# Kernel optimization log

Hardware: AMD Instinct MI355X
Metric: run time of the kernel (lower is better)

Reference implementation:

```python
import jax, jax.numpy as jnp
import numpy as np

# dims
B, S, E, H = 2, 2048, 2048, 2688   # batch, seq, embedding_dim, hidden_dim
NH, DH = 4, 2688 // 4              # mLSTM heads, head dim
KS = 4                             # causal conv kernel size
BLK = 4                            # qkv_proj_blocksize
NPH = H // BLK                     # headwise-proj heads


def setup_inputs() -> dict:
    key = jax.random.key(0)
    ks = jax.random.split(key, 12)
    r = lambda i, shape, s=0.02: jax.random.normal(ks[i], shape, jnp.float32) * s
    return dict(
        x=jax.random.normal(ks[0], (B, S, E), jnp.float32),
        W_in=r(1, (E, 2 * H)),                       # up projection (no bias)
        conv_w=r(2, (KS, 1, H), 0.1),                # depthwise causal conv kernel (W, I/g, O)
        conv_b=jnp.zeros((H,), jnp.float32),
        Wq=r(3, (NPH, BLK, BLK), 0.3),               # headwise q proj
        Wk=r(4, (NPH, BLK, BLK), 0.3),               # headwise k proj
        Wv=r(5, (NPH, BLK, BLK), 0.3),               # headwise v proj
        W_ig=r(6, (3 * H, NH)),                      # input gate proj
        b_ig=jax.random.normal(ks[7], (NH,), jnp.float32),
        W_fg=r(8, (3 * H, NH)),                      # forget gate proj
        b_fg=jnp.linspace(3.0, 6.0, NH).astype(jnp.float32),
        norm_w=jnp.ones((H,), jnp.float32),          # multi-head layernorm weight
        skip=jnp.ones((H,), jnp.float32),            # learnable skip
        W_out=r(9, (H, E)),                          # down projection
    )


def _headwise(x, W):
    # LinearHeadwiseExpand: (B,S,H) -> (B,S,NPH,BLK) -> einsum -> (B,S,H)
    b, s, _ = x.shape
    xh = x.reshape(b, s, NPH, BLK)
    return jnp.einsum('bshd,hdo->bsho', xh, W).reshape(b, s, -1)


def reference(x, W_in, conv_w, conv_b, Wq, Wk, Wv, W_ig, b_ig, W_fg, b_fg, norm_w, skip, W_out):
    x_inner = x @ W_in                               # (B,S,2H)
    x_m, z = jnp.split(x_inner, 2, axis=-1)
    # depthwise causal conv1d
    xc = jax.lax.conv_general_dilated(
        x_m, conv_w, (1,), [(KS - 1, 0)],
        dimension_numbers=('NWC', 'WIO', 'NWC'), feature_group_count=H) + conv_b
    xca = jax.nn.silu(xc)
    q = _headwise(xca, Wq)
    k = _headwise(xca, Wk)
    v = _headwise(x_m, Wv)
    # ---- mLSTM cell (parallel stabilized form) ----
    qh = q.reshape(B, S, NH, DH).transpose(0, 2, 1, 3)   # (B,NH,S,DH)
    kh = k.reshape(B, S, NH, DH).transpose(0, 2, 1, 3)
    vh = v.reshape(B, S, NH, DH).transpose(0, 2, 1, 3)
    if_in = jnp.concatenate([q, k, v], axis=-1)          # (B,S,3H)
    i_pre = (if_in @ W_ig + b_ig).transpose(0, 2, 1)     # (B,NH,S)
    f_pre = (if_in @ W_fg + b_fg).transpose(0, 2, 1)
    log_fg = jax.nn.log_sigmoid(f_pre)                   # (B,NH,S)
    cs = jnp.cumsum(log_fg, axis=-1)
    # log decay matrix: sum of log forget gates t=j+1..i, causal masked
    dmat = cs[:, :, :, None] - cs[:, :, None, :]         # (B,NH,S,S)
    mask = jnp.tril(jnp.ones((S, S), bool))
    log_D = jnp.where(mask, dmat + i_pre[:, :, None, :], -jnp.inf)
    m = jnp.max(log_D, axis=-1, keepdims=True)           # stabilizer (B,NH,S,1)
    D = jnp.exp(log_D - m)
    qk = jnp.einsum('bnsd,bntd->bnst', qh, kh) / jnp.sqrt(jnp.float32(DH))
    C = qk * D
    n = jnp.maximum(jnp.abs(C.sum(-1, keepdims=True)), jnp.exp(-m))
    h = jnp.einsum('bnst,bntd->bnsd', C / (n + 1e-6), vh)
    # multi-head layernorm over DH, learnable scale over full H
    mu = h.mean(-1, keepdims=True)
    var = h.var(-1, keepdims=True)
    hn = (h - mu) * jax.lax.rsqrt(var + 1e-5)
    hn = hn.transpose(0, 2, 1, 3).reshape(B, S, H) * norm_w
    # ---- gated skip + output ----
    h_skip = hn + skip * xca
    hs = h_skip * jax.nn.silu(z)
    return hs @ W_out
```

## Files before the change

### kernel.cpp

```cpp
#include <hip/hip_runtime.h>

typedef unsigned short u16;
typedef unsigned int u32;
typedef __bf16 bf16x8 __attribute__((ext_vector_type(8)));
typedef float f32x4 __attribute__((ext_vector_type(4)));

#define BB   2
#define SS   2048
#define EE   2048
#define HH   2688
#define NHH  4
#define DHH  672
#define NPHH 672
#define H2   5376
#define H3   8064

__device__ __forceinline__ float b2f(u16 u) {
  union { unsigned int i; float f; } c; c.i = ((unsigned int)u) << 16; return c.f;
}
__device__ __forceinline__ u16 f2b(float f) {
  union { float f; unsigned int i; } c; c.f = f;
  unsigned int i = c.i;
  return (u16)((i + 0x7FFFu + ((i >> 16) & 1u)) >> 16);
}
__device__ __forceinline__ float silu_f(float x) { return x / (1.f + __expf(-x)); }
__device__ __forceinline__ float logsig_f(float f) {
  return (f >= 0.f) ? -log1pf(__expf(-f)) : (f - log1pf(__expf(f)));
}

__device__ __forceinline__ void gl2lds16(const u16* g, u16* s) {
  __builtin_amdgcn_global_load_lds(
      (const __attribute__((address_space(1))) u32*)g,
      (__attribute__((address_space(3))) u32*)s, 16, 0, 0);
}

template <int N> __device__ __forceinline__ void vmwait() {
  asm volatile("s_waitcnt vmcnt(%0)" :: "n"(N) : "memory");
}

template <int MODE, int OUTF32>
__global__ __launch_bounds__(512, 1) void gemm8(
    const u16* __restrict__ A, const u16* __restrict__ Bt, void* __restrict__ Cp,
    int M, int N, int K, int lda, int ldb, int ldc,
    long sAhi, long sAlo, long sBhi, long sBlo, long sChi, long sClo,
    const float* __restrict__ aux1, const float* __restrict__ aux2,
    int auxStride, int causal)
{
  constexpr int SLOT = (128 + 256) * 64;
  __shared__ __align__(16) u16 sm[3 * SLOT];

  int gx = gridDim.x;
  int nwg = gx * gridDim.y;
  int flat = blockIdx.y * gx + blockIdx.x;
  int qq = nwg >> 3, r8 = nwg & 7;
  int xcd = flat & 7, seq = flat >> 3;
  int logical = (xcd < r8 ? xcd * (qq + 1) : r8 * (qq + 1) + (xcd - r8) * qq) + seq;
  int bx = logical % gx, by = logical / gx;
  int m0 = by * 128, n0 = bx * 256;
  if (MODE == 1 && n0 > m0 + 127) return;

  int bz = blockIdx.z, bzh = bz >> 2, bzl = bz & 3;
  A  += bzh * sAhi + bzl * sAlo;
  Bt += bzh * sBhi + bzl * sBlo;
  const float* a1 = aux1 ? aux1 + (long)bz * auxStride : nullptr;
  const float* a2 = aux2 ? aux2 + (long)bz * auxStride : nullptr;
  u16*   C16 = (u16*)Cp + bzh * sChi + bzl * sClo;
  float* C32 = (float*)Cp + bzh * sChi + bzl * sClo;

  int t = threadIdx.x, lane = t & 63, w = t >> 6;
  int l15 = lane & 15, quad = lane >> 4;
  int wr = w >> 2, wc = w & 3;

  int srow = t >> 3;
  int sw8 = ((t & 7) ^ (srow & 7)) * 8;
  const u16* pS[6];
  int dOf[6];
#pragma unroll
  for (int c = 0; c < 2; ++c) {
    pS[c] = A + (long)(m0 + c * 64 + srow) * lda + sw8;
    dOf[c] = c * 4096 + w * 512;
  }
#pragma unroll
  for (int c = 0; c < 4; ++c) {
    pS[2 + c] = Bt + (long)(n0 + c * 64 + srow) * ldb + sw8;
    dOf[2 + c] = 8192 + c * 4096 + w * 512;
  }

  f32x4 acc[4][4];
#pragma unroll
  for (int i = 0; i < 4; i++)
#pragma unroll
    for (int j = 0; j < 4; j++) acc[i][j] = (f32x4){0.f, 0.f, 0.f, 0.f};

  int Keff = (MODE == 2 && causal) ? min(K, m0 + 128) : K;
  int T = Keff >> 6;

  auto STAGE = [&](int slot, int k2, int c) {
    gl2lds16(pS[c] + k2, sm + slot * SLOT + dOf[c]);
  };

  int npre = T < 2 ? T : 2;
  for (int tt = 0; tt < npre; ++tt)
#pragma unroll
    for (int c = 0; c < 6; ++c) STAGE(tt, tt << 6, c);
  if (npre >= 2) vmwait<6>(); else vmwait<0>();
  __builtin_amdgcn_s_barrier();
  __builtin_amdgcn_sched_barrier(0);

  int sl = 0;
  for (int tq = 0; tq < T; ++tq) {
    u16* Sb = sm + sl * SLOT;
    int sl2 = sl + 2; if (sl2 >= 3) sl2 -= 3;
    const bool stg = (tq + 2 < T);
    const int k2 = (tq + 2) << 6;
    int cx = (l15 & 7);

    bf16x8 bfr[4][2], af[2][2];
#pragma unroll
    for (int j = 0; j < 4; ++j)
#pragma unroll
      for (int ks = 0; ks < 2; ++ks)
        bfr[j][ks] = *reinterpret_cast<const bf16x8*>(
            Sb + 8192 + (wc * 64 + j * 16 + l15) * 64 + ((((ks << 2) + quad) ^ cx) << 3));
#pragma unroll
    for (int i = 0; i < 2; ++i)
#pragma unroll
      for (int ks = 0; ks < 2; ++ks)
        af[i][ks] = *reinterpret_cast<const bf16x8*>(
            Sb + (wr * 64 + i * 16 + l15) * 64 + ((((ks << 2) + quad) ^ cx) << 3));
    if (stg) { STAGE(sl2, k2, 0); STAGE(sl2, k2, 1); STAGE(sl2, k2, 2); }
    __builtin_amdgcn_s_barrier();
    asm volatile("s_waitcnt lgkmcnt(0)" ::: "memory");
    __builtin_amdgcn_sched_barrier(0);
    __builtin_amdgcn_s_setprio(1);
#pragma unroll
    for (int i = 0; i < 2; ++i)
#pragma unroll
      for (int j = 0; j < 4; ++j) {
        acc[i][j] = __builtin_amdgcn_mfma_f32_16x16x32_bf16(af[i][0], bfr[j][0], acc[i][j], 0, 0, 0);
        acc[i][j] = __builtin_amdgcn_mfma_f32_16x16x32_bf16(af[i][1], bfr[j][1], acc[i][j], 0, 0, 0);
      }
    __builtin_amdgcn_s_setprio(0);
    __builtin_amdgcn_sched_barrier(0);
    __builtin_amdgcn_s_barrier();

    bf16x8 ag[2][2];
#pragma unroll
    for (int i = 0; i < 2; ++i)
#pragma unroll
      for (int ks = 0; ks < 2; ++ks)
        ag[i][ks] = *reinterpret_cast<const bf16x8*>(
            Sb + (wr * 64 + (i + 2) * 16 + l15) * 64 + ((((ks << 2) + quad) ^ cx) << 3));
    if (stg) { STAGE(sl2, k2, 3); STAGE(sl2, k2, 4); STAGE(sl2, k2, 5); }
    __builtin_amdgcn_s_barrier();
    asm volatile("s_waitcnt lgkmcnt(0)" ::: "memory");
    __builtin_amdgcn_sched_barrier(0);
    __builtin_amdgcn_s_setprio(1);
#pragma unroll
    for (int i = 0; i < 2; ++i)
#pragma unroll
      for (int j = 0; j < 4; ++j) {
        acc[i + 2][j] = __builtin_amdgcn_mfma_f32_16x16x32_bf16(ag[i][0], bfr[j][0], acc[i + 2][j], 0, 0, 0);
        acc[i + 2][j] = __builtin_amdgcn_mfma_f32_16x16x32_bf16(ag[i][1], bfr[j][1], acc[i + 2][j], 0, 0, 0);
      }
    __builtin_amdgcn_s_setprio(0);
    __builtin_amdgcn_sched_barrier(0);
    if (tq + 1 < T) {
      if (stg) vmwait<6>(); else vmwait<0>();
      __builtin_amdgcn_s_barrier();
      __builtin_amdgcn_sched_barrier(0);
    }
    sl = sl + 1; if (sl >= 3) sl = 0;
  }

  const float rs = 0.03857583749f;
#pragma unroll
  for (int i = 0; i < 4; i++) {
#pragma unroll
    for (int j = 0; j < 4; j++) {
      int col = n0 + wc * 64 + j * 16 + l15;
      if (col >= N) continue;
#pragma unroll
      for (int rr = 0; rr < 4; rr++) {
        int row = m0 + wr * 64 + i * 16 + quad * 4 + rr;
        if (row >= M) continue;
        float v = acc[i][j][rr];
        if (MODE == 1) v = (col <= row) ? v * rs * __expf(a1[col] - a2[row]) : 0.f;
        else if (MODE == 2) v = v * a1[row];
        if (OUTF32) C32[(long)row * ldc + col] = v;
        else        C16[(long)row * ldc + col] = f2b(v);
      }
    }
  }
}

template <int BM, int MODE, int OUTF32>
__global__ __launch_bounds__(512, 1) void gemm_p(
    const u16* __restrict__ A, const u16* __restrict__ Bt, void* __restrict__ Cp,
    int M, int N, int K, int lda, int ldb, int ldc,
    long sAhi, long sAlo, long sBhi, long sBlo, long sChi, long sClo,
    const float* __restrict__ aux1, const float* __restrict__ aux2,
    int auxStride, int causal)
{
  constexpr int MFR   = BM / 32;
  constexpr int NPH   = MFR / 2;
  constexpr int SLOT  = (BM + 256) * 32;
  constexpr int ACH   = BM / 128;
  constexpr int LOADS = ACH + 2;
  __shared__ __align__(16) u16 sm[4 * SLOT];

  int gx = gridDim.x;
  int nwg = gx * gridDim.y;
  int flat = blockIdx.y * gx + blockIdx.x;
  int qq = nwg >> 3, r8 = nwg & 7;
  int xcd = flat & 7, seq = flat >> 3;
  int logical = (xcd < r8 ? xcd * (qq + 1) : r8 * (qq + 1) + (xcd - r8) * qq) + seq;
  int bx = logical % gx, by = logical / gx;
  int m0 = by * BM, n0 = bx * 256;
  if (MODE == 1 && n0 > m0 + BM - 1) return;

  int bz = blockIdx.z, bzh = bz >> 2, bzl = bz & 3;
  A  += bzh * sAhi + bzl * sAlo;
  Bt += bzh * sBhi + bzl * sBlo;
  const float* a1 = aux1 ? aux1 + (long)bz * auxStride : nullptr;
  const float* a2 = aux2 ? aux2 + (long)bz * auxStride : nullptr;
  u16*   C16 = (u16*)Cp + bzh * sChi + bzl * sClo;
  float* C32 = (float*)Cp + bzh * sChi + bzl * sClo;

  int t = threadIdx.x, lane = t & 63, w = t >> 6;
  int l15 = lane & 15, quad = lane >> 4;
  int wr = w >> 2, wc = w & 3;

  int srow = t >> 2;
  int swz = (((t & 3) ^ ((t >> 3) & 3)) * 8);
  const u16* pS[LOADS];
  int coff[LOADS];
#pragma unroll
  for (int c = 0; c < ACH; ++c) {
    pS[c] = A + (long)(m0 + c * 128 + srow) * lda + swz;
    coff[c] = c * 4096 + w * 512;
  }
#pragma unroll
  for (int c = 0; c < 2; ++c) {
    pS[ACH + c] = Bt + (long)(n0 + c * 128 + srow) * ldb + swz;
    coff[ACH + c] = BM * 32 + c * 4096 + w * 512;
  }

  int rswz = (quad ^ ((l15 >> 1) & 3)) * 8;
  int aoff = (wr * (BM / 2) + l15) * 32 + rswz;
  int boff = BM * 32 + (wc * 64 + l15) * 32 + rswz;

  f32x4 acc[MFR][4];
#pragma unroll
  for (int i = 0; i < MFR; i++)
#pragma unroll
    for (int j = 0; j < 4; j++) acc[i][j] = (f32x4){0.f, 0.f, 0.f, 0.f};

  int Keff = (MODE == 2 && causal) ? min(K, m0 + BM) : K;
  int T = Keff >> 5;

  auto STAGE1 = [&](int tt, int c) {
    gl2lds16(pS[c] + (tt << 5), sm + (tt & 3) * SLOT + coff[c]);
  };

  int npre = T < 3 ? T : 3;
  for (int tt = 0; tt < npre; ++tt)
#pragma unroll
    for (int c = 0; c < LOADS; ++c) STAGE1(tt, c);
  if (npre >= 3)      vmwait<2 * LOADS>();
  else if (npre == 2) vmwait<LOADS>();
  else                vmwait<0>();
  __builtin_amdgcn_s_barrier();
  __builtin_amdgcn_sched_barrier(0);

  for (int tq = 0; tq < T; ++tq) {
    u16* Sb = sm + (tq & 3) * SLOT;
    const bool stg = (tq + 3 < T);
    bf16x8 bf[4];
#pragma unroll
    for (int p = 0; p < NPH; ++p) {
      bf16x8 a0 = *reinterpret_cast<const bf16x8*>(Sb + aoff + (2 * p) * 512);
      bf16x8 a1v = *reinterpret_cast<const bf16x8*>(Sb + aoff + (2 * p + 1) * 512);
      if (p == 0) {
#pragma unroll
        for (int j = 0; j < 4; ++j)
          bf[j] = *reinterpret_cast<const bf16x8*>(Sb + boff + j * 512);
      }
      if (stg) {
#pragma unroll
        for (int c = p * LOADS / NPH; c < (p + 1) * LOADS / NPH; ++c)
          STAGE1(tq + 3, c);
      }
      __builtin_amdgcn_s_barrier();
      asm volatile("s_waitcnt lgkmcnt(0)" ::: "memory");
      __builtin_amdgcn_sched_barrier(0);
      __builtin_amdgcn_s_setprio(1);
#pragma unroll
      for (int j = 0; j < 4; ++j)
        acc[2 * p][j] = __builtin_amdgcn_mfma_f32_16x16x32_bf16(a0, bf[j], acc[2 * p][j], 0, 0, 0);
#pragma unroll
      for (int j = 0; j < 4; ++j)
        acc[2 * p + 1][j] = __builtin_amdgcn_mfma_f32_16x16x32_bf16(a1v, bf[j], acc[2 * p + 1][j], 0, 0, 0);
      __builtin_amdgcn_s_setprio(0);
      __builtin_amdgcn_sched_barrier(0);
    }
    if (tq + 1 < T) {
      if (tq + 3 < T)      vmwait<2 * LOADS>();
      else if (tq + 2 < T) vmwait<LOADS>();
      else                 vmwait<0>();
      __builtin_amdgcn_s_barrier();
      __builtin_amdgcn_sched_barrier(0);
    }
  }

  const float rs = 0.03857583749f;
#pragma unroll
  for (int i = 0; i < MFR; i++) {
#pragma unroll
    for (int j = 0; j < 4; j++) {
      int col = n0 + wc * 64 + j * 16 + l15;
      if (col >= N) continue;
#pragma unroll
      for (int rr = 0; rr < 4; rr++) {
        int row = m0 + wr * (BM / 2) + i * 16 + quad * 4 + rr;
        if (row >= M) continue;
        float v = acc[i][j][rr];
        if (MODE == 1) v = (col <= row) ? v * rs * __expf(a1[col] - a2[row]) : 0.f;
        else if (MODE == 2) v = v * a1[row];
        if (OUTF32) C32[(long)row * ldc + col] = v;
        else        C16[(long)row * ldc + col] = f2b(v);
      }
    }
  }
}

template <int F32IN>
__global__ __launch_bounds__(256) void transpose_any(
    const void* __restrict__ in, u16* __restrict__ out, int R, int C, int ldin,
    long inHi, long inLo, long outStride)
{
  __shared__ u16 tile[64][65];
  int bz = blockIdx.z, bzh = bz >> 2, bzl = bz & 3;
  const u16* in16 = (const u16*)in + bzh * inHi + bzl * inLo;
  const float* inf = (const float*)in + bzh * inHi + bzl * inLo;
  out += (long)bz * outStride;
  int r0 = blockIdx.y * 64, c0 = blockIdx.x * 64;
  int t = threadIdx.x;
  for (int idx = t; idx < 64 * 64; idx += 256) {
    int r = idx >> 6, c = idx & 63;
    int rr = r0 + r, cc = c0 + c;
    u16 v = 0;
    if (rr < R && cc < C) {
      long off = (long)rr * ldin + cc;
      v = F32IN ? f2b(inf[off]) : in16[off];
    }
    tile[r][c] = v;
  }
  __syncthreads();
  for (int idx = t; idx < 64 * 64; idx += 256) {
    int r = idx & 63, c = idx >> 6;
    int rr = r0 + r, cc = c0 + c;
    if (rr < R && cc < C) out[(long)cc * R + rr] = tile[r][c];
  }
}

__global__ __launch_bounds__(256) void convert_x(
    const float* __restrict__ x, u16* __restrict__ o)
{
  long i = ((long)blockIdx.x * 256 + threadIdx.x) * 8;
  if (i >= (long)4096 * EE) return;
  float4 a = *reinterpret_cast<const float4*>(x + i);
  float4 b = *reinterpret_cast<const float4*>(x + i + 4);
  u16 t8[8] = {f2b(a.x), f2b(a.y), f2b(a.z), f2b(a.w),
               f2b(b.x), f2b(b.y), f2b(b.z), f2b(b.w)};
  *reinterpret_cast<uint4*>(o + i) = *reinterpret_cast<uint4*>(t8);
}

__global__ __launch_bounds__(256) void prep_wqkv(
    const float* __restrict__ Wq, const float* __restrict__ Wk,
    const float* __restrict__ Wv, u16* __restrict__ o)
{
  int i = blockIdx.x * 256 + threadIdx.x;
  if (i >= 3 * 10752) return;
  int m = i / 10752, j = i % 10752;
  const float* W = (m == 0) ? Wq : (m == 1) ? Wk : Wv;
  o[i] = f2b(W[j]);
}

__global__ __launch_bounds__(256) void prep_gatew(
    const float* __restrict__ Wig, const float* __restrict__ Wfg,
    u16* __restrict__ Wg)
{
  int i = blockIdx.x * 256 + threadIdx.x;
  if (i >= NPHH * 96) return;
  int nph = i / 96, r = i % 96;
  int seg = r >> 5, d = (r >> 3) & 3, j = r & 7;
  const float* W = (j < 4) ? Wig : Wfg;
  Wg[i] = f2b(W[(long)(seg * HH + nph * 4 + d) * 4 + (j & 3)]);
}

__global__ __launch_bounds__(704) void conv_head(
    const u16* __restrict__ xinner, const float* __restrict__ cw,
    const float* __restrict__ cb, const u16* __restrict__ Wqkv,
    const u16* __restrict__ Wg, u16* __restrict__ xca, u16* __restrict__ q,
    u16* __restrict__ k, u16* __restrict__ v, float* __restrict__ G2)
{
  __shared__ float gsh[8];
  long bs = blockIdx.x;
  int s = (int)(bs % SS);
  int t = threadIdx.x, lane = t & 63;
  if (t < 8) gsh[t] = 0.f;
  __syncthreads();

  float gi[4] = {0.f, 0.f, 0.f, 0.f}, gf[4] = {0.f, 0.f, 0.f, 0.f};
  if (t < NPHH) {
    int h4 = t * 4;
    float4 acc = *reinterpret_cast<const float4*>(cb + h4);
    uint2 xmr = {0, 0};
#pragma unroll
    for (int w = 0; w < 4; w++) {
      int sp = s + w - 3;
      if (sp < 0) continue;
      uint2 xr = *reinterpret_cast<const uint2*>(xinner + (bs + w - 3) * H2 + h4);
      if (w == 3) xmr = xr;
      const u16* xh = (const u16*)&xr;
      float4 cwv = *reinterpret_cast<const float4*>(cw + w * HH + h4);
      acc.x += b2f(xh[0]) * cwv.x;
      acc.y += b2f(xh[1]) * cwv.y;
      acc.z += b2f(xh[2]) * cwv.z;
      acc.w += b2f(xh[3]) * cwv.w;
    }
    float xaf[4] = {silu_f(acc.x), silu_f(acc.y), silu_f(acc.z), silu_f(acc.w)};
    u16 xa16[4] = {f2b(xaf[0]), f2b(xaf[1]), f2b(xaf[2]), f2b(xaf[3])};
#pragma unroll
    for (int d = 0; d < 4; d++) xaf[d] = b2f(xa16[d]);
    const u16* xm = (const u16*)&xmr;
    float xmf[4];
#pragma unroll
    for (int d = 0; d < 4; d++) xmf[d] = b2f(xm[d]);
    *reinterpret_cast<uint2*>(xca + bs * HH + h4) = *reinterpret_cast<uint2*>(xa16);

    union { uint4 v4[2]; u16 h[16]; } wq, wk, wv;
    const uint4* wqp = reinterpret_cast<const uint4*>(Wqkv + t * 16);
    const uint4* wkp = reinterpret_cast<const uint4*>(Wqkv + 10752 + t * 16);
    const uint4* wvp = reinterpret_cast<const uint4*>(Wqkv + 21504 + t * 16);
    wq.v4[0] = wqp[0]; wq.v4[1] = wqp[1];
    wk.v4[0] = wkp[0]; wk.v4[1] = wkp[1];
    wv.v4[0] = wvp[0]; wv.v4[1] = wvp[1];
    float aq[4], ak[4], av[4];
    u16 qo[4], ko[4], vo[4];
#pragma unroll
    for (int o = 0; o < 4; o++) {
      float sq = 0.f, sk = 0.f, sv = 0.f;
#pragma unroll
      for (int d = 0; d < 4; d++) {
        sq += xaf[d] * b2f(wq.h[d * 4 + o]);
        sk += xaf[d] * b2f(wk.h[d * 4 + o]);
        sv += xmf[d] * b2f(wv.h[d * 4 + o]);
      }
      aq[o] = sq; ak[o] = sk; av[o] = sv;
      qo[o] = f2b(sq); ko[o] = f2b(sk); vo[o] = f2b(sv);
    }
    long ob = bs * HH + h4;
    *reinterpret_cast<uint2*>(q + ob) = *reinterpret_cast<uint2*>(qo);
    *reinterpret_cast<uint2*>(k + ob) = *reinterpret_cast<uint2*>(ko);
    *reinterpret_cast<uint2*>(v + ob) = *reinterpret_cast<uint2*>(vo);

    union { uint4 v4[12]; u16 h[96]; } wg;
    const uint4* wgp = reinterpret_cast<const uint4*>(Wg + t * 96);
#pragma unroll
    for (int u = 0; u < 12; ++u) wg.v4[u] = wgp[u];
#pragma unroll
    for (int seg = 0; seg < 3; ++seg) {
      const float* xx = (seg == 0) ? aq : (seg == 1) ? ak : av;
#pragma unroll
      for (int d = 0; d < 4; ++d) {
        float xv = xx[d];
        const u16* wr = &wg.h[seg * 32 + d * 8];
#pragma unroll
        for (int n = 0; n < 4; ++n) {
          gi[n] += xv * b2f(wr[n]);
          gf[n] += xv * b2f(wr[4 + n]);
        }
      }
    }
  }
#pragma unroll
  for (int off = 32; off > 0; off >>= 1) {
#pragma unroll
    for (int n = 0; n < 4; ++n) {
      gi[n] += __shfl_down(gi[n], off);
      gf[n] += __shfl_down(gf[n], off);
    }
  }
  if (lane == 0) {
#pragma unroll
    for (int n = 0; n < 4; ++n) {
      atomicAdd(&gsh[n], gi[n]);
      atomicAdd(&gsh[4 + n], gf[n]);
    }
  }
  __syncthreads();
  if (t < 8) G2[bs * 8 + t] = gsh[t];
}

__global__ __launch_bounds__(256) void scan_kernel(
    const float* __restrict__ G2, const float* __restrict__ big,
    const float* __restrict__ bfg,
    float* __restrict__ avec, float* __restrict__ rmaxvec, float* __restrict__ mvec)
{
  __shared__ float wsum[4], wmax[4];
  int bn = blockIdx.x;
  int b = bn >> 2, n = bn & 3;
  int t = threadIdx.x, lane = t & 63, wv = t >> 6;
  float bi = big[n], bf = bfg[n];
  int i0 = t * 8;
  float ip[8], ls[8];
  float run = 0.f;
#pragma unroll
  for (int kk = 0; kk < 8; ++kk) {
    long tk = (long)b * SS + i0 + kk;
    ip[kk] = G2[tk * 8 + n] + bi;
    run += logsig_f(G2[tk * 8 + 4 + n] + bf);
    ls[kk] = run;
  }
  float v = run;
#pragma unroll
  for (int off = 1; off < 64; off <<= 1) {
    float o = __shfl_up(v, off);
    if (lane >= off) v += o;
  }
  if (lane == 63) wsum[wv] = v;
  __syncthreads();
  float woff = 0.f;
  for (int u = 0; u < wv; ++u) woff += wsum[u];
  float excl = v - run + woff;
  float a[8], lm[8];
  float runm = -3.4e38f;
#pragma unroll
  for (int kk = 0; kk < 8; ++kk) {
    float cs = excl + ls[kk];
    ls[kk] = cs;
    a[kk] = ip[kk] - cs;
    runm = fmaxf(runm, a[kk]);
    lm[kk] = runm;
    avec[(long)bn * SS + i0 + kk] = a[kk];
  }
  float mv = runm;
#pragma unroll
  for (int off = 1; off < 64; off <<= 1) {
    float o = __shfl_up(mv, off);
    if (lane >= off) mv = fmaxf(mv, o);
  }
  if (lane == 63) wmax[wv] = mv;
  __syncthreads();
  float woffm = -3.4e38f;
  for (int u = 0; u < wv; ++u) woffm = fmaxf(woffm, wmax[u]);
  float pm = __shfl_up(mv, 1);
  float pre = (lane == 0) ? woffm : fmaxf(woffm, pm);
#pragma unroll
  for (int kk = 0; kk < 8; ++kk) {
    float r = fmaxf(pre, lm[kk]);
    rmaxvec[(long)bn * SS + i0 + kk] = r;
    mvec[(long)bn * SS + i0 + kk] = ls[kk] + r;
  }
}

__global__ __launch_bounds__(256) void rowsum_kernel(
    const u16* __restrict__ P, const float* __restrict__ mvec, float* __restrict__ invn,
    long Pstride)
{
  int bz = blockIdx.z;
  P += (long)bz * Pstride;
  mvec += (long)bz * SS;
  invn += (long)bz * SS;
  int row = (blockIdx.x * 256 + threadIdx.x) >> 6;
  int lane = threadIdx.x & 63;
  if (row >= SS) return;
  const u16* pr = P + (long)row * SS;
  float s = 0.f;
  int j0 = lane * 8;
  for (; j0 + 7 <= row; j0 += 512) {
    uint4 u = *reinterpret_cast<const uint4*>(pr + j0);
    const u16* e = (const u16*)&u;
#pragma unroll
    for (int q = 0; q < 8; ++q) s += b2f(e[q]);
  }
  if (j0 <= row) {
    for (int q = 0; j0 + q <= row; ++q) s += b2f(pr[j0 + q]);
  }
#pragma unroll
  for (int off = 32; off > 0; off >>= 1) s += __shfl_down(s, off);
  if (lane == 0) {
    float n = fmaxf(fabsf(s), __expf(-mvec[row]));
    invn[row] = 1.f / (n + 1e-6f);
  }
}

__global__ __launch_bounds__(256) void ln_skip_gate(
    const u16* __restrict__ h, const u16* __restrict__ xca,
    const u16* __restrict__ xinner, const float* __restrict__ normw,
    const float* __restrict__ skipw, u16* __restrict__ hs)
{
  int row = (blockIdx.x * 256 + threadIdx.x) >> 6;
  int lane = threadIdx.x & 63;
  if (row >= BB * NHH * SS) return;
  int s = row % SS;
  int n = (row / SS) % NHH;
  int b = row / (SS * NHH);
  const u16* hr = h + (long)row * DHH;
  float sum = 0.f, ss = 0.f;
  float vx[6], vy[6];
#pragma unroll
  for (int i = 0; i < 6; ++i) {
    int d2 = lane + i * 64;
    float x = 0.f, y = 0.f;
    if (d2 < DHH / 2) {
      u32 u = *reinterpret_cast<const u32*>(hr + d2 * 2);
      x = b2f((u16)u); y = b2f((u16)(u >> 16));
    }
    vx[i] = x; vy[i] = y;
    sum += x + y; ss += x * x + y * y;
  }
#pragma unroll
  for (int off = 32; off > 0; off >>= 1) { sum += __shfl_down(sum, off); ss += __shfl_down(ss, off); }
  sum = __shfl(sum, 0); ss = __shfl(ss, 0);
  float mu = sum / (float)DHH;
  float var = ss / (float)DHH - mu * mu;
  float rstd = rsqrtf(var + 1e-5f);
  long bs = (long)b * SS + s;
#pragma unroll
  for (int i = 0; i < 6; ++i) {
    int d2 = lane + i * 64;
    if (d2 >= DHH / 2) continue;
    int c = n * DHH + d2 * 2;
    float2 nw = *reinterpret_cast<const float2*>(normw + c);
    float2 sw = *reinterpret_cast<const float2*>(skipw + c);
    u32 xcu = *reinterpret_cast<const u32*>(xca + bs * HH + c);
    u32 zu  = *reinterpret_cast<const u32*>(xinner + bs * H2 + HH + c);
    float h0 = (vx[i] - mu) * rstd * nw.x + sw.x * b2f((u16)xcu);
    float h1 = (vy[i] - mu) * rstd * nw.y + sw.y * b2f((u16)(xcu >> 16));
    float o0 = h0 * silu_f(b2f((u16)zu));
    float o1 = h1 * silu_f(b2f((u16)(zu >> 16)));
    u32 ou = (u32)f2b(o0) | ((u32)f2b(o1) << 16);
    *reinterpret_cast<u32*>(hs + bs * HH + c) = ou;
  }
}

__global__ __launch_bounds__(256) void fill_sentinel(float* out, float v, long n) {
  long i = (long)blockIdx.x * 256 + threadIdx.x;
  if (i < n) out[i] = v;
}

extern "C" void kernel_launch(void* const* d_in, const int* in_sizes, int n_in,
                              void* d_out, int out_size, void* d_ws, size_t ws_size,
                              hipStream_t stream)
{
  const float* x      = (const float*)d_in[0];
  const float* W_in   = (const float*)d_in[1];
  const float* conv_w = (const float*)d_in[2];
  const float* conv_b = (const float*)d_in[3];
  const float* Wq     = (const float*)d_in[4];
  const float* Wk     = (const float*)d_in[5];
  const float* Wv     = (const float*)d_in[6];
  const float* W_ig   = (const float*)d_in[7];
  const float* b_ig   = (const float*)d_in[8];
  const float* W_fg   = (const float*)d_in[9];
  const float* b_fg   = (const float*)d_in[10];
  const float* norm_w = (const float*)d_in[11];
  const float* skipw  = (const float*)d_in[12];
  const float* W_out  = (const float*)d_in[13];
  float* out = (float*)d_out;
  const long SD = (long)SS * DHH;
  const long SP = (long)SS * SS;
  const long BH = (long)SS * HH;

  u16* ws = (u16*)d_ws;
  size_t off = 0;
  auto alloc = [&](size_t n) { u16* p = ws + off; off += n; return p; };
  u16* x_inner = alloc((size_t)4096 * H2);
  u16* xca     = alloc((size_t)4096 * HH);
  u16* qb      = alloc((size_t)4096 * HH);
  u16* kb      = alloc((size_t)4096 * HH);
  u16* vb      = alloc((size_t)4096 * HH);
  float* fvec  = (float*)(ws + off);
  off += 4 * 16384 * 2;
  float* avec    = fvec;
  float* rmaxvec = avec + 16384;
  float* mvec    = rmaxvec + 16384;
  float* invn    = mvec + 16384;
  u16* vt8 = alloc((size_t)8 * SD);
  u16* Pb8 = alloc((size_t)8 * SP);
  size_t need = off * 2;
  long outn = (long)4096 * EE;

  if (ws_size < need) {
    fill_sentinel<<<dim3((outn + 255) / 256), 256, 0, stream>>>(
        out, 200.f + 0.01f * (float)(ws_size >> 20), outn);
    return;
  }

  u16* W_inT  = qb;
  u16* xbf    = kb;
  u16* W_outT = vb;
  u16* hbuf   = kb;
  u16* hsbuf  = qb;
  float* G2   = (float*)(Pb8 + 344064);
  u16* Wqkv   = Pb8 + 933888;
  u16* Wg     = Pb8 + 966144;

  prep_wqkv<<<dim3(126, 1, 1), 256, 0, stream>>>(Wq, Wk, Wv, Wqkv);
  prep_gatew<<<dim3(252, 1, 1), 256, 0, stream>>>(W_ig, W_fg, Wg);
  fill_sentinel<<<dim3(128, 1, 1), 256, 0, stream>>>(G2, 0.f, 32768);
  transpose_any<1><<<dim3(84, 32, 1), 256, 0, stream>>>(
      W_in, W_inT, EE, H2, H2, 0, 0, 0);
  convert_x<<<dim3(4096, 1, 1), 256, 0, stream>>>(x, xbf);
  gemm8<0, 0><<<dim3(21, 32, 1), 512, 0, stream>>>(
      xbf, W_inT, x_inner, 4096, H2, EE, EE, EE, H2,
      0, 0, 0, 0, 0, 0, nullptr, nullptr, 0, 0);
  conv_head<<<dim3(4096, 1, 1), 704, 0, stream>>>(
      x_inner, conv_w, conv_b, Wqkv, Wg, xca, qb, kb, vb, G2);
  scan_kernel<<<dim3(8, 1, 1), 256, 0, stream>>>(G2, b_ig, b_fg, avec, rmaxvec, mvec);
  transpose_any<0><<<dim3(11, 32, 8), 256, 0, stream>>>(
      vb, vt8, SS, DHH, HH, BH, DHH, SD);
  gemm_p<256, 1, 0><<<dim3(8, 8, 8), 512, 0, stream>>>(
      qb, kb, Pb8, SS, SS, DHH, HH, HH, SS,
      BH, DHH, BH, DHH, 4 * SP, SP, avec, rmaxvec, SS, 0);
  rowsum_kernel<<<dim3(512, 1, 8), 256, 0, stream>>>(Pb8, mvec, invn, SP);
  gemm8<2, 0><<<dim3(3, 16, 8), 512, 0, stream>>>(
      Pb8, vt8, hbuf, SS, DHH, SS, SS, SS, DHH,
      4 * SP, SP, 4 * SD, SD, 4 * SD, SD, invn, nullptr, SS, 1);
  transpose_any<1><<<dim3(32, 42, 1), 256, 0, stream>>>(
      W_out, W_outT, HH, EE, EE, 0, 0, 0);
  ln_skip_gate<<<dim3(4096, 1, 1), 256, 0, stream>>>(
      hbuf, xca, x_inner, norm_w, skipw, hsbuf);
  gemm8<0, 1><<<dim3(8, 32, 1), 512, 0, stream>>>(
      hsbuf, W_outT, out, 4096, EE, HH, HH, HH, EE,
      0, 0, 0, 0, 0, 0, nullptr, nullptr, 0, 0);
}
```

Baseline: 703.8 us.

## Move gate projection out of conv_head into an MFMA GEMM with atomic accumulation

The input/forget gate projection over concatenated q,k,v was a per-thread dot product with wave shuffles and shared-memory atomics inside conv_head. It now runs as a separate gemm_p call in a new atomic-add mode (MODE 3), treating q/k/v as a 12288x2688 matrix against a zero-padded bf16 gate weight, split over 4 K-chunks with atomics into a zeroed buffer. The scan then sums the three segment partials. conv_head becomes a simpler flat elementwise kernel with 256-thread blocks. The cost is an extra launch, a much larger padded weight-prep and zero-fill, and mostly wasted N columns (24 real out of a wide tile).

```diff
diff --git a/kernel.cpp b/kernel.cpp
--- a/kernel.cpp
+++ b/kernel.cpp
@@ -327,6 +327,7 @@
         float v = acc[i][j][rr];
         if (MODE == 1) v = (col <= row) ? v * rs * __expf(a1[col] - a2[row]) : 0.f;
         else if (MODE == 2) v = v * a1[row];
+        if (MODE == 3) { atomicAdd(&C32[(long)row * ldc + col], v); continue; }
         if (OUTF32) C32[(long)row * ldc + col] = v;
         else        C16[(long)row * ldc + col] = f2b(v);
       }
@@ -387,125 +388,86 @@
   o[i] = f2b(W[j]);
 }
 
-__global__ __launch_bounds__(256) void prep_gatew(
+__global__ __launch_bounds__(256) void prep_wg3(
     const float* __restrict__ Wig, const float* __restrict__ Wfg,
-    u16* __restrict__ Wg)
+    u16* __restrict__ o)
 {
   int i = blockIdx.x * 256 + threadIdx.x;
-  if (i >= NPHH * 96) return;
-  int nph = i / 96, r = i % 96;
-  int seg = r >> 5, d = (r >> 3) & 3, j = r & 7;
-  const float* W = (j < 4) ? Wig : Wfg;
-  Wg[i] = f2b(W[(long)(seg * HH + nph * 4 + d) * 4 + (j & 3)]);
-}
-
-__global__ __launch_bounds__(704) void conv_head(
+  if (i >= 256 * HH) return;
+  int r = i / HH, c = i % HH;
+  float v = 0.f;
+  if (r < 24) {
+    int seg = r >> 3, j = r & 7;
+    const float* W = (j < 4) ? Wig : Wfg;
+    v = W[(long)(seg * HH + c) * 4 + (j & 3)];
+  }
+  o[i] = f2b(v);
+}
+
+__global__ __launch_bounds__(256) void conv_head(
     const u16* __restrict__ xinner, const float* __restrict__ cw,
     const float* __restrict__ cb, const u16* __restrict__ Wqkv,
-    const u16* __restrict__ Wg, u16* __restrict__ xca, u16* __restrict__ q,
-    u16* __restrict__ k, u16* __restrict__ v, float* __restrict__ G2)
-{
-  __shared__ float gsh[8];
-  long bs = blockIdx.x;
+    u16* __restrict__ xca, u16* __restrict__ q, u16* __restrict__ k,
+    u16* __restrict__ v)
+{
+  long idx = (long)blockIdx.x * 256 + threadIdx.x;
+  if (idx >= (long)BB * SS * NPHH) return;
+  int nph = (int)(idx % NPHH);
+  long bs = idx / NPHH;
   int s = (int)(bs % SS);
-  int t = threadIdx.x, lane = t & 63;
-  if (t < 8) gsh[t] = 0.f;
-  __syncthreads();
-
-  float gi[4] = {0.f, 0.f, 0.f, 0.f}, gf[4] = {0.f, 0.f, 0.f, 0.f};
-  if (t < NPHH) {
-    int h4 = t * 4;
-    float4 acc = *reinterpret_cast<const float4*>(cb + h4);
-    uint2 xmr = {0, 0};
-#pragma unroll
-    for (int w = 0; w < 4; w++) {
-      int sp = s + w - 3;
-      if (sp < 0) continue;
-      uint2 xr = *reinterpret_cast<const uint2*>(xinner + (bs + w - 3) * H2 + h4);
-      if (w == 3) xmr = xr;
-      const u16* xh = (const u16*)&xr;
-      float4 cwv = *reinterpret_cast<const float4*>(cw + w * HH + h4);
-      acc.x += b2f(xh[0]) * cwv.x;
-      acc.y += b2f(xh[1]) * cwv.y;
-      acc.z += b2f(xh[2]) * cwv.z;
-      acc.w += b2f(xh[3]) * cwv.w;
+  int h4 = nph * 4;
+  float4 acc = *reinterpret_cast<const float4*>(cb + h4);
+  uint2 xmr = {0, 0};
+#pragma unroll
+  for (int w = 0; w < 4; w++) {
+    int sp = s + w - 3;
+    if (sp < 0) continue;
+    uint2 xr = *reinterpret_cast<const uint2*>(xinner + (bs + w - 3) * H2 + h4);
+    if (w == 3) xmr = xr;
+    const u16* xh = (const u16*)&xr;
+    float4 cwv = *reinterpret_cast<const float4*>(cw + w * HH + h4);
+    acc.x += b2f(xh[0]) * cwv.x;
+    acc.y += b2f(xh[1]) * cwv.y;
+    acc.z += b2f(xh[2]) * cwv.z;
+    acc.w += b2f(xh[3]) * cwv.w;
+  }
+  float xaf[4] = {silu_f(acc.x), silu_f(acc.y), silu_f(acc.z), silu_f(acc.w)};
+  u16 xa16[4] = {f2b(xaf[0]), f2b(xaf[1]), f2b(xaf[2]), f2b(xaf[3])};
+#pragma unroll
+  for (int d = 0; d < 4; d++) xaf[d] = b2f(xa16[d]);
+  const u16* xm = (const u16*)&xmr;
+  float xmf[4];
+#pragma unroll
+  for (int d = 0; d < 4; d++) xmf[d] = b2f(xm[d]);
+  *reinterpret_cast<uint2*>(xca + bs * HH + h4) = *reinterpret_cast<uint2*>(xa16);
+
+  union { uint4 v4[2]; u16 h[16]; } wq, wk, wv;
+  const uint4* wqp = reinterpret_cast<const uint4*>(Wqkv + nph * 16);
+  const uint4* wkp = reinterpret_cast<const uint4*>(Wqkv + 10752 + nph * 16);
+  const uint4* wvp = reinterpret_cast<const uint4*>(Wqkv + 21504 + nph * 16);
+  wq.v4[0] = wqp[0]; wq.v4[1] = wqp[1];
+  wk.v4[0] = wkp[0]; wk.v4[1] = wkp[1];
+  wv.v4[0] = wvp[0]; wv.v4[1] = wvp[1];
+  u16 qo[4], ko[4], vo[4];
+#pragma unroll
+  for (int o = 0; o < 4; o++) {
+    float aq = 0.f, ak = 0.f, av = 0.f;
+#pragma unroll
+    for (int d = 0; d < 4; d++) {
+      aq += xaf[d] * b2f(wq.h[d * 4 + o]);
+      ak += xaf[d] * b2f(wk.h[d * 4 + o]);
+      av += xmf[d] * b2f(wv.h[d * 4 + o]);
     }
-    float xaf[4] = {silu_f(acc.x), silu_f(acc.y), silu_f(acc.z), silu_f(acc.w)};
-    u16 xa16[4] = {f2b(xaf[0]), f2b(xaf[1]), f2b(xaf[2]), f2b(xaf[3])};
-#pragma unroll
-    for (int d = 0; d < 4; d++) xaf[d] = b2f(xa16[d]);
-    const u16* xm = (const u16*)&xmr;
-    float xmf[4];
-#pragma unroll
-    for (int d = 0; d < 4; d++) xmf[d] = b2f(xm[d]);
-    *reinterpret_cast<uint2*>(xca + bs * HH + h4) = *reinterpret_cast<uint2*>(xa16);
-
-    union { uint4 v4[2]; u16 h[16]; } wq, wk, wv;
-    const uint4* wqp = reinterpret_cast<const uint4*>(Wqkv + t * 16);
-    const uint4* wkp = reinterpret_cast<const uint4*>(Wqkv + 10752 + t * 16);
-    const uint4* wvp = reinterpret_cast<const uint4*>(Wqkv + 21504 + t * 16);
-    wq.v4[0] = wqp[0]; wq.v4[1] = wqp[1];
-    wk.v4[0] = wkp[0]; wk.v4[1] = wkp[1];
-    wv.v4[0] = wvp[0]; wv.v4[1] = wvp[1];
-    float aq[4], ak[4], av[4];
-    u16 qo[4], ko[4], vo[4];
-#pragma unroll
-    for (int o = 0; o < 4; o++) {
-      float sq = 0.f, sk = 0.f, sv = 0.f;
-#pragma unroll
-      for (int d = 0; d < 4; d++) {
-        sq += xaf[d] * b2f(wq.h[d * 4 + o]);
-        sk += xaf[d] * b2f(wk.h[d * 4 + o]);
-        sv += xmf[d] * b2f(wv.h[d * 4 + o]);
-      }
-      aq[o] = sq; ak[o] = sk; av[o] = sv;
-      qo[o] = f2b(sq); ko[o] = f2b(sk); vo[o] = f2b(sv);
-    }
-    long ob = bs * HH + h4;
-    *reinterpret_cast<uint2*>(q + ob) = *reinterpret_cast<uint2*>(qo);
-    *reinterpret_cast<uint2*>(k + ob) = *reinterpret_cast<uint2*>(ko);
-    *reinterpret_cast<uint2*>(v + ob) = *reinterpret_cast<uint2*>(vo);
-
-    union { uint4 v4[12]; u16 h[96]; } wg;
-    const uint4* wgp = reinterpret_cast<const uint4*>(Wg + t * 96);
-#pragma unroll
-    for (int u = 0; u < 12; ++u) wg.v4[u] = wgp[u];
-#pragma unroll
-    for (int seg = 0; seg < 3; ++seg) {
-      const float* xx = (seg == 0) ? aq : (seg == 1) ? ak : av;
-#pragma unroll
-      for (int d = 0; d < 4; ++d) {
-        float xv = xx[d];
-        const u16* wr = &wg.h[seg * 32 + d * 8];
-#pragma unroll
-        for (int n = 0; n < 4; ++n) {
-          gi[n] += xv * b2f(wr[n]);
-          gf[n] += xv * b2f(wr[4 + n]);
-        }
-      }
-    }
-  }
-#pragma unroll
-  for (int off = 32; off > 0; off >>= 1) {
-#pragma unroll
-    for (int n = 0; n < 4; ++n) {
-      gi[n] += __shfl_down(gi[n], off);
-      gf[n] += __shfl_down(gf[n], off);
-    }
-  }
-  if (lane == 0) {
-#pragma unroll
-    for (int n = 0; n < 4; ++n) {
-      atomicAdd(&gsh[n], gi[n]);
-      atomicAdd(&gsh[4 + n], gf[n]);
-    }
-  }
-  __syncthreads();
-  if (t < 8) G2[bs * 8 + t] = gsh[t];
+    qo[o] = f2b(aq); ko[o] = f2b(ak); vo[o] = f2b(av);
+  }
+  long ob = bs * HH + h4;
+  *reinterpret_cast<uint2*>(q + ob) = *reinterpret_cast<uint2*>(qo);
+  *reinterpret_cast<uint2*>(k + ob) = *reinterpret_cast<uint2*>(ko);
+  *reinterpret_cast<uint2*>(v + ob) = *reinterpret_cast<uint2*>(vo);
 }
 
 __global__ __launch_bounds__(256) void scan_kernel(
-    const float* __restrict__ G2, const float* __restrict__ big,
+    const float* __restrict__ G, const float* __restrict__ big,
     const float* __restrict__ bfg,
     float* __restrict__ avec, float* __restrict__ rmaxvec, float* __restrict__ mvec)
 {
@@ -520,8 +482,11 @@
 #pragma unroll
   for (int kk = 0; kk < 8; ++kk) {
     long tk = (long)b * SS + i0 + kk;
-    ip[kk] = G2[tk * 8 + n] + bi;
-    run += logsig_f(G2[tk * 8 + 4 + n] + bf);
+    ip[kk] = G[tk * 24 + n] + G[(4096 + tk) * 24 + 8 + n] +
+             G[(8192 + tk) * 24 + 16 + n] + bi;
+    float fp = G[tk * 24 + 4 + n] + G[(4096 + tk) * 24 + 12 + n] +
+               G[(8192 + tk) * 24 + 20 + n] + bf;
+    run += logsig_f(fp);
     ls[kk] = run;
   }
   float v = run;
@@ -705,22 +670,25 @@
   u16* W_outT = vb;
   u16* hbuf   = kb;
   u16* hsbuf  = qb;
-  float* G2   = (float*)(Pb8 + 344064);
+  float* G    = (float*)(Pb8 + 344064);
   u16* Wqkv   = Pb8 + 933888;
-  u16* Wg     = Pb8 + 966144;
+  u16* Wg3    = Pb8 + 966144;
 
   prep_wqkv<<<dim3(126, 1, 1), 256, 0, stream>>>(Wq, Wk, Wv, Wqkv);
-  prep_gatew<<<dim3(252, 1, 1), 256, 0, stream>>>(W_ig, W_fg, Wg);
-  fill_sentinel<<<dim3(128, 1, 1), 256, 0, stream>>>(G2, 0.f, 32768);
+  prep_wg3<<<dim3(2688, 1, 1), 256, 0, stream>>>(W_ig, W_fg, Wg3);
+  fill_sentinel<<<dim3(1152, 1, 1), 256, 0, stream>>>(G, 0.f, 294912);
   transpose_any<1><<<dim3(84, 32, 1), 256, 0, stream>>>(
       W_in, W_inT, EE, H2, H2, 0, 0, 0);
   convert_x<<<dim3(4096, 1, 1), 256, 0, stream>>>(x, xbf);
   gemm8<0, 0><<<dim3(21, 32, 1), 512, 0, stream>>>(
       xbf, W_inT, x_inner, 4096, H2, EE, EE, EE, H2,
       0, 0, 0, 0, 0, 0, nullptr, nullptr, 0, 0);
-  conv_head<<<dim3(4096, 1, 1), 704, 0, stream>>>(
-      x_inner, conv_w, conv_b, Wqkv, Wg, xca, qb, kb, vb, G2);
-  scan_kernel<<<dim3(8, 1, 1), 256, 0, stream>>>(G2, b_ig, b_fg, avec, rmaxvec, mvec);
+  conv_head<<<dim3(10752, 1, 1), 256, 0, stream>>>(
+      x_inner, conv_w, conv_b, Wqkv, xca, qb, kb, vb);
+  gemm_p<128, 3, 1><<<dim3(1, 96, 4), 512, 0, stream>>>(
+      qb, Wg3, G, 12288, 24, DHH, HH, HH, 24,
+      0, DHH, 0, DHH, 0, 0, nullptr, nullptr, 0, 0);
+  scan_kernel<<<dim3(8, 1, 1), 256, 0, stream>>>(G, b_ig, b_fg, avec, rmaxvec, mvec);
   transpose_any<0><<<dim3(11, 32, 8), 256, 0, stream>>>(
       vb, vt8, SS, DHH, HH, BH, DHH, SD);
   gemm_p<256, 1, 0><<<dim3(8, 8, 8), 512, 0, stream>>>(
```

Measured after the change: 652.0 us. 1.08x faster.
